# Kernel tuning notes

Measured on AMD Instinct MI355X. Metric: run time of the kernel, lower is better.

The kernel has to match this reference:

```python
import jax, jax.numpy as jnp
import numpy as np

N_NODES = 50000
N_EDGES = 1_000_000
D = 256


def gcn_conv(x, src, dst, ew, W, b, n):
    # PyG GCNConv with edge_weight: linear transform, add self-loops (w=1),
    # symmetric normalization deg^{-1/2} w deg^{-1/2}, scatter-sum, + bias.
    x = x @ W  # (n, out)
    loop = jnp.arange(n)
    src_l = jnp.concatenate([src, loop])
    dst_l = jnp.concatenate([dst, loop])
    ew_l = jnp.concatenate([ew, jnp.ones((n,), ew.dtype)])
    deg = jax.ops.segment_sum(ew_l, dst_l, num_segments=n)
    dinv = jnp.where(deg > 0, jax.lax.rsqrt(deg), 0.0).astype(x.dtype)
    norm = dinv[src_l] * ew_l * dinv[dst_l]  # (E+n,)
    out = jax.ops.segment_sum(norm[:, None] * x[src_l], dst_l, num_segments=n)
    return out + b


def setup_inputs() -> dict:
    key = jax.random.key(0)
    k = jax.random.split(key, 8)
    glorot = 1.0 / np.sqrt(D)
    return {
        "x": jax.random.normal(k[0], (N_NODES, D), jnp.float32),
        "edge_index": jax.random.randint(k[1], (2, N_EDGES), 0, N_NODES, jnp.int64),
        "edge_weight": jax.random.uniform(k[2], (N_EDGES,), jnp.float32),
        "W1": jax.random.normal(k[3], (D, D), jnp.float32) * glorot,
        "b1": jnp.zeros((D,), jnp.float32),
        "W2": jax.random.normal(k[4], (D, D), jnp.float32) * glorot,
        "b2": jnp.zeros((D,), jnp.float32),
    }


def reference(x, edge_index, edge_weight, W1, b1, W2, b2):
    n = x.shape[0]
    src, dst = edge_index[0], edge_index[1]
    h = gcn_conv(x, src, dst, edge_weight, W1, b1, n)
    h = jax.nn.relu(h)  # dropout is identity at eval
    out = gcn_conv(h, src, dst, edge_weight, W2, b2, n)
    return out
```

## Files before the change

### kernel.cpp

```cpp
#include <hip/hip_runtime.h>
#include <hip/hip_bf16.h>
#include <stdint.h>


#define D 256
#define CAP 64

typedef __attribute__((ext_vector_type(8))) short short8;
typedef __attribute__((ext_vector_type(4))) float floatx4;

__device__ inline unsigned short f2bf_rne(float f) {
    union { float f; uint32_t u; } v; v.f = f;
    uint32_t u = v.u;
    return (unsigned short)((u + 0x7FFFu + ((u >> 16) & 1u)) >> 16);
}
__device__ inline float bf_lo(uint32_t u) { union { uint32_t u; float f; } v; v.u = u << 16; return v.f; }
__device__ inline float bf_hi(uint32_t u) { union { uint32_t u; float f; } v; v.u = u & 0xFFFF0000u; return v.f; }

#define FXS 16777216.0f

#define GBM 128
#define GBN 128
#define GBK 32
#define LDA 40
#define NB_CVT 64
#define NB_P1 1600

__device__ void gemm1_block(const float* __restrict__ x, const float* __restrict__ W1,
                            unsigned short* __restrict__ C, int n, int bid,
                            unsigned char* smem) {
    unsigned short (*As)[LDA] = (unsigned short(*)[LDA])smem;
    unsigned short (*Bs)[LDA] = (unsigned short(*)[LDA])(smem + GBM * LDA * 2);
    int t = threadIdx.x;
    int bm = (bid >> 1) * GBM;
    int bn = (bid & 1) * GBN;
    int w = t >> 6, l = t & 63;
    int wm = (w >> 1) * 64, wn = (w & 1) * 64;
    int lr = l & 15;
    int lq = l >> 4;
    floatx4 acc[4][4] = {};
    for (int k0 = 0; k0 < D; k0 += GBK) {
        #pragma unroll
        for (int i = 0; i < 2; i++) {
            int c = t + i * 256;
            int row = c >> 2;
            int kk = (c & 3) * 8;
            int gr = bm + row;
            short8 av = {};
            if (gr < n) {
                const float* ap = x + (size_t)gr * D + k0 + kk;
                float4 f0 = *(const float4*)ap;
                float4 f1 = *(const float4*)(ap + 4);
                av[0] = (short)f2bf_rne(f0.x); av[1] = (short)f2bf_rne(f0.y);
                av[2] = (short)f2bf_rne(f0.z); av[3] = (short)f2bf_rne(f0.w);
                av[4] = (short)f2bf_rne(f1.x); av[5] = (short)f2bf_rne(f1.y);
                av[6] = (short)f2bf_rne(f1.z); av[7] = (short)f2bf_rne(f1.w);
            }
            *(short8*)&As[row][kk] = av;
        }
        #pragma unroll
        for (int i = 0; i < 4; i++) {
            int idx = t + i * 256;
            int kk = idx >> 5;
            int nn4 = (idx & 31) << 2;
            float4 wv = *(const float4*)(W1 + (size_t)(k0 + kk) * D + bn + nn4);
            Bs[nn4 + 0][kk] = f2bf_rne(wv.x);
            Bs[nn4 + 1][kk] = f2bf_rne(wv.y);
            Bs[nn4 + 2][kk] = f2bf_rne(wv.z);
            Bs[nn4 + 3][kk] = f2bf_rne(wv.w);
        }
        __syncthreads();
        short8 af[4], bfr[4];
        #pragma unroll
        for (int i = 0; i < 4; i++) af[i] = *(const short8*)&As[wm + i * 16 + lr][lq * 8];
        #pragma unroll
        for (int j = 0; j < 4; j++) bfr[j] = *(const short8*)&Bs[wn + j * 16 + lr][lq * 8];
        #pragma unroll
        for (int i = 0; i < 4; i++)
            #pragma unroll
            for (int j = 0; j < 4; j++)
                acc[i][j] = __builtin_amdgcn_mfma_f32_16x16x32_bf16(af[i], bfr[j], acc[i][j], 0, 0, 0);
        __syncthreads();
    }
    #pragma unroll
    for (int i = 0; i < 4; i++) {
        #pragma unroll
        for (int r = 0; r < 4; r++) {
            int row = bm + wm + i * 16 + lq * 4 + r;
            if (row >= n) continue;
            #pragma unroll
            for (int j = 0; j < 4; j++) {
                int col = bn + wn + j * 16 + lr;
                C[(size_t)row * D + col] = f2bf_rne(acc[i][j][r]);
            }
        }
    }
}

__device__ void cvtw2_block(const float* __restrict__ W2, unsigned short* __restrict__ Wt,
                            int bid, unsigned char* smem) {
    float (*sw)[33] = (float(*)[33])smem;
    int k0 = (bid >> 3) * 32, n0 = (bid & 7) * 32;
    int t = threadIdx.x;
    int tx = t & 31, ty0 = (t >> 5) * 4;
    #pragma unroll
    for (int r = 0; r < 4; r++)
        sw[ty0 + r][tx] = W2[(size_t)(k0 + ty0 + r) * D + n0 + tx];
    __syncthreads();
    #pragma unroll
    for (int r = 0; r < 4; r++)
        Wt[(size_t)(n0 + ty0 + r) * D + k0 + tx] = f2bf_rne(sw[tx][ty0 + r]);
}

__device__ void pass1_block(const int* __restrict__ src, const int* __restrict__ dst,
                            const float* __restrict__ ew,
                            unsigned long long* __restrict__ packed,
                            uint2* __restrict__ edata, int E, int bid, int nb) {
    int stride = nb * 256;
    for (int e = bid * 256 + threadIdx.x; e < E; e += stride) {
        int d = dst[e];
        float w = ew[e];
        uint32_t fx = __float2uint_rn(w * FXS);
        unsigned long long old =
            atomicAdd(&packed[(size_t)d << 3], ((unsigned long long)fx << 32) | 1ull);
        uint32_t r = (uint32_t)old;
        if (r < CAP) {
            uint2 v; v.x = (uint32_t)src[e]; v.y = __float_as_uint(w);
            edata[((size_t)d << 6) + r] = v;
        }
    }
}

__global__ __launch_bounds__(256) void fused1_kernel(const float* __restrict__ x,
                                                     const float* __restrict__ W1,
                                                     const float* __restrict__ W2,
                                                     const int* __restrict__ src,
                                                     const int* __restrict__ dst,
                                                     const float* __restrict__ ew,
                                                     unsigned short* __restrict__ xws,
                                                     unsigned short* __restrict__ w2t,
                                                     unsigned long long* __restrict__ packed,
                                                     uint2* __restrict__ edata,
                                                     int n, int E, int nb_gemm) {
    __shared__ unsigned char smem[2 * GBM * LDA * 2];
    int bid = blockIdx.x;
    if (bid < nb_gemm) {
        gemm1_block(x, W1, xws, n, bid, smem);
    } else if (bid < nb_gemm + NB_CVT) {
        cvtw2_block(W2, w2t, bid - nb_gemm, smem);
    } else {
        pass1_block(src, dst, ew, packed, edata, E, bid - nb_gemm - NB_CVT, NB_P1);
    }
}

__global__ void unpack_kernel(const unsigned long long* __restrict__ packed,
                              float* __restrict__ dinv, int n) {
    int i = blockIdx.x * 256 + threadIdx.x;
    if (i < n) {
        float deg = (float)(packed[(size_t)i << 3] >> 32) * (1.0f / FXS) + 1.0f;
        dinv[i] = rsqrtf(deg);
    }
}

__global__ __launch_bounds__(256) void gemm2_kernel(const unsigned short* __restrict__ A,
                                                    const unsigned short* __restrict__ Bt,
                                                    unsigned short* __restrict__ C, int n) {
    __shared__ unsigned short As[GBM][LDA];
    __shared__ unsigned short Bs[GBN][LDA];
    int t = threadIdx.x;
    int bm = blockIdx.x * GBM;
    int bn = blockIdx.y * GBN;
    int w = t >> 6, l = t & 63;
    int wm = (w >> 1) * 64, wn = (w & 1) * 64;
    int lr = l & 15;
    int lq = l >> 4;
    floatx4 acc[4][4] = {};
    for (int k0 = 0; k0 < D; k0 += GBK) {
        #pragma unroll
        for (int i = 0; i < 2; i++) {
            int c = t + i * 256;
            int row = c >> 2;
            int kk = (c & 3) * 8;
            int gr = bm + row;
            short8 av = {};
            if (gr < n) av = *(const short8*)&A[(size_t)gr * D + k0 + kk];
            *(short8*)&As[row][kk] = av;
            short8 bv = *(const short8*)&Bt[(size_t)(bn + row) * D + k0 + kk];
            *(short8*)&Bs[row][kk] = bv;
        }
        __syncthreads();
        short8 af[4], bfr[4];
        #pragma unroll
        for (int i = 0; i < 4; i++) af[i] = *(const short8*)&As[wm + i * 16 + lr][lq * 8];
        #pragma unroll
        for (int j = 0; j < 4; j++) bfr[j] = *(const short8*)&Bs[wn + j * 16 + lr][lq * 8];
        #pragma unroll
        for (int i = 0; i < 4; i++)
            #pragma unroll
            for (int j = 0; j < 4; j++)
                acc[i][j] = __builtin_amdgcn_mfma_f32_16x16x32_bf16(af[i], bfr[j], acc[i][j], 0, 0, 0);
        __syncthreads();
    }
    #pragma unroll
    for (int i = 0; i < 4; i++) {
        #pragma unroll
        for (int r = 0; r < 4; r++) {
            int row = bm + wm + i * 16 + lq * 4 + r;
            if (row >= n) continue;
            #pragma unroll
            for (int j = 0; j < 4; j++) {
                int col = bn + wn + j * 16 + lr;
                C[(size_t)row * D + col] = f2bf_rne(acc[i][j][r]);
            }
        }
    }
}

template <bool RELU, bool OUT_BF16>
__global__ __launch_bounds__(256) void gather_kernel(const unsigned short* __restrict__ xw,
                                                     const uint2* __restrict__ edata,
                                                     const unsigned long long* __restrict__ packed,
                                                     const float* __restrict__ dinv,
                                                     const float* __restrict__ bias,
                                                     void* __restrict__ outv, int n) {
    int wid = threadIdx.x >> 6;
    int lane = threadIdx.x & 63;
    int node = (blockIdx.x << 2) + wid;
    if (node >= n) return;
    int half = lane >> 5;
    int cl = lane & 31;
    int ch = cl << 3;
    float di = dinv[node];

    float acc[8];
    {
        uint4 r = *(const uint4*)(xw + (size_t)node * D + ch);
        float4 b0 = *(const float4*)(bias + ch);
        float4 b1 = *(const float4*)(bias + ch + 4);
        float ws = (half == 0) ? di * di : 0.0f;
        float bs = (half == 0) ? 1.0f : 0.0f;
        acc[0] = ws * bf_lo(r.x) + bs * b0.x;
        acc[1] = ws * bf_hi(r.x) + bs * b0.y;
        acc[2] = ws * bf_lo(r.y) + bs * b0.z;
        acc[3] = ws * bf_hi(r.y) + bs * b0.w;
        acc[4] = ws * bf_lo(r.z) + bs * b1.x;
        acc[5] = ws * bf_hi(r.z) + bs * b1.y;
        acc[6] = ws * bf_lo(r.w) + bs * b1.z;
        acc[7] = ws * bf_hi(r.w) + bs * b1.w;
    }

    int cnt = (int)(uint32_t)packed[(size_t)node << 3];
    cnt = min(cnt, CAP);
    const uint2* ebase = edata + ((size_t)node << 6);

    for (int j = 0; j < cnt; j += 8) {
        #pragma unroll
        for (int k = 0; k < 4; k++) {
            int e = j + 2 * k + half;
            bool valid = e < cnt;
            uint2 m; m.x = (uint32_t)node; m.y = 0u;
            if (valid) m = ebase[e];
            float co = dinv[m.x] * __uint_as_float(m.y) * di;
            uint4 r = *(const uint4*)(xw + (size_t)m.x * D + ch);
            acc[0] += co * bf_lo(r.x);
            acc[1] += co * bf_hi(r.x);
            acc[2] += co * bf_lo(r.y);
            acc[3] += co * bf_hi(r.y);
            acc[4] += co * bf_lo(r.z);
            acc[5] += co * bf_hi(r.z);
            acc[6] += co * bf_lo(r.w);
            acc[7] += co * bf_hi(r.w);
        }
    }
    #pragma unroll
    for (int k = 0; k < 8; k++) acc[k] += __shfl_xor(acc[k], 32);

    if (RELU) {
        #pragma unroll
        for (int k = 0; k < 8; k++) acc[k] = fmaxf(acc[k], 0.0f);
    }
    if (OUT_BF16) {
        if (half == 0) {
            uint4 o;
            o.x = (uint32_t)f2bf_rne(acc[0]) | ((uint32_t)f2bf_rne(acc[1]) << 16);
            o.y = (uint32_t)f2bf_rne(acc[2]) | ((uint32_t)f2bf_rne(acc[3]) << 16);
            o.z = (uint32_t)f2bf_rne(acc[4]) | ((uint32_t)f2bf_rne(acc[5]) << 16);
            o.w = (uint32_t)f2bf_rne(acc[6]) | ((uint32_t)f2bf_rne(acc[7]) << 16);
            *(uint4*)((unsigned short*)outv + (size_t)node * D + ch) = o;
        }
    } else {
        float4 o;
        int b = half * 4;
        o.x = acc[b + 0]; o.y = acc[b + 1]; o.z = acc[b + 2]; o.w = acc[b + 3];
        *(float4*)((float*)outv + (size_t)node * D + ch + b) = o;
    }
}

extern "C" void kernel_launch(void* const* d_in, const int* in_sizes, int n_in,
                              void* d_out, int out_size, void* d_ws, size_t ws_size,
                              hipStream_t stream) {
    const float* x  = (const float*)d_in[0];
    const int*   ei = (const int*)d_in[1];
    const float* ew = (const float*)d_in[2];
    const float* W1 = (const float*)d_in[3];
    const float* b1 = (const float*)d_in[4];
    const float* W2 = (const float*)d_in[5];
    const float* b2 = (const float*)d_in[6];
    float* out = (float*)d_out;

    const int n = in_sizes[0] / D;
    const int E = in_sizes[2];
    const int* src = ei;
    const int* dst = ei + E;

    char* ws = (char*)d_ws;
    size_t off = 0;
    auto carve = [&](size_t bytes) {
        char* p = ws + off;
        off = (off + bytes + 255) & ~(size_t)255;
        return p;
    };
    unsigned long long* packed = (unsigned long long*)carve((size_t)n * 64);
    float*          dinv = (float*)carve((size_t)n * 4);
    uint2*          edata = (uint2*)carve((size_t)n * CAP * 8);
    unsigned short* w2t  = (unsigned short*)carve((size_t)D * D * 2);
    unsigned short* xws  = (unsigned short*)carve((size_t)n * D * 2);
    unsigned short* hb   = (unsigned short*)carve((size_t)n * D * 2);

    const int nb_gemm = ((n + GBM - 1) / GBM) * 2;
    const int nb_node = (n + 255) / 256;

    (void)hipMemsetAsync(packed, 0, (size_t)n * 64, stream);

    fused1_kernel<<<nb_gemm + NB_CVT + NB_P1, 256, 0, stream>>>(
        x, W1, W2, src, dst, ew, xws, w2t, packed, edata, n, E, nb_gemm);

    unpack_kernel<<<nb_node, 256, 0, stream>>>(packed, dinv, n);

    dim3 agrid((n + 3) / 4);
    gather_kernel<true, true><<<agrid, 256, 0, stream>>>(xws, edata, packed, dinv, b1, hb, n);

    dim3 ggrid((n + GBM - 1) / GBM, D / GBN);
    gemm2_kernel<<<ggrid, 256, 0, stream>>>(hb, w2t, xws, n);

    gather_kernel<false, false><<<agrid, 256, 0, stream>>>(xws, edata, packed, dinv, b2, out, n);
}
```

Baseline: 362.9 us.

## Swizzle GEMM block order, vectorize W1 staging, use nontemporal stores

GEMM blocks are remapped so that groups of eight M-tiles are visited with both N-halves in sequence, which should improve L2 reuse, and gemm2 moves to a 1D grid to match. The W1 tile load now reads four rows per thread and writes packed bf16 pairs to shared memory as one 64-bit store, replacing four scalar transposed stores. Edge-data writes in pass1 and the final fp32 output writes use nontemporal stores to limit cache pollution. The risk is that strided W1 reads coalesce less well, and the nontemporal edge stores may evict data that the gather kernels later reread.

```diff
diff --git a/kernel.cpp b/kernel.cpp
--- a/kernel.cpp
+++ b/kernel.cpp
@@ -26,14 +26,30 @@
 #define NB_CVT 64
 #define NB_P1 1600
 
+__device__ inline void gemm_bmbn(int lin, int nbm, int& bm, int& bn) {
+    int full = (nbm >> 3) << 4;
+    if (lin < full) {
+        int q = lin >> 4, r = lin & 15;
+        bm = q * 8 + (r & 7);
+        bn = r >> 3;
+    } else {
+        int rr = lin - full;
+        bm = (full >> 1) + (rr >> 1);
+        bn = rr & 1;
+    }
+}
+
 __device__ void gemm1_block(const float* __restrict__ x, const float* __restrict__ W1,
                             unsigned short* __restrict__ C, int n, int bid,
                             unsigned char* smem) {
     unsigned short (*As)[LDA] = (unsigned short(*)[LDA])smem;
     unsigned short (*Bs)[LDA] = (unsigned short(*)[LDA])(smem + GBM * LDA * 2);
     int t = threadIdx.x;
-    int bm = (bid >> 1) * GBM;
-    int bn = (bid & 1) * GBN;
+    int nbm = (n + GBM - 1) / GBM;
+    int bmi, bni;
+    gemm_bmbn(bid, nbm, bmi, bni);
+    int bm = bmi * GBM;
+    int bn = bni * GBN;
     int w = t >> 6, l = t & 63;
     int wm = (w >> 1) * 64, wn = (w & 1) * 64;
     int lr = l & 15;
@@ -60,14 +76,18 @@
         }
         #pragma unroll
         for (int i = 0; i < 4; i++) {
-            int idx = t + i * 256;
-            int kk = idx >> 5;
-            int nn4 = (idx & 31) << 2;
-            float4 wv = *(const float4*)(W1 + (size_t)(k0 + kk) * D + bn + nn4);
-            Bs[nn4 + 0][kk] = f2bf_rne(wv.x);
-            Bs[nn4 + 1][kk] = f2bf_rne(wv.y);
-            Bs[nn4 + 2][kk] = f2bf_rne(wv.z);
-            Bs[nn4 + 3][kk] = f2bf_rne(wv.w);
+            int gidx = t + i * 256;
+            int nn = gidx & 127;
+            int kk = (gidx >> 7) << 2;
+            const float* wp = W1 + (size_t)(k0 + kk) * D + bn + nn;
+            float w0 = wp[0];
+            float w1 = wp[D];
+            float w2 = wp[2 * D];
+            float w3 = wp[3 * D];
+            uint32_t p0 = (uint32_t)f2bf_rne(w0) | ((uint32_t)f2bf_rne(w1) << 16);
+            uint32_t p1 = (uint32_t)f2bf_rne(w2) | ((uint32_t)f2bf_rne(w3) << 16);
+            uint2 pv; pv.x = p0; pv.y = p1;
+            *(uint2*)&Bs[nn][kk] = pv;
         }
         __syncthreads();
         short8 af[4], bfr[4];
@@ -115,7 +135,7 @@
 __device__ void pass1_block(const int* __restrict__ src, const int* __restrict__ dst,
                             const float* __restrict__ ew,
                             unsigned long long* __restrict__ packed,
-                            uint2* __restrict__ edata, int E, int bid, int nb) {
+                            unsigned long long* __restrict__ edata, int E, int bid, int nb) {
     int stride = nb * 256;
     for (int e = bid * 256 + threadIdx.x; e < E; e += stride) {
         int d = dst[e];
@@ -125,8 +145,9 @@
             atomicAdd(&packed[(size_t)d << 3], ((unsigned long long)fx << 32) | 1ull);
         uint32_t r = (uint32_t)old;
         if (r < CAP) {
-            uint2 v; v.x = (uint32_t)src[e]; v.y = __float_as_uint(w);
-            edata[((size_t)d << 6) + r] = v;
+            unsigned long long pv =
+                ((unsigned long long)__float_as_uint(w) << 32) | (uint32_t)src[e];
+            __builtin_nontemporal_store(pv, &edata[((size_t)d << 6) + r]);
         }
     }
 }
@@ -140,7 +161,7 @@
                                                      unsigned short* __restrict__ xws,
                                                      unsigned short* __restrict__ w2t,
                                                      unsigned long long* __restrict__ packed,
-                                                     uint2* __restrict__ edata,
+                                                     unsigned long long* __restrict__ edata,
                                                      int n, int E, int nb_gemm) {
     __shared__ unsigned char smem[2 * GBM * LDA * 2];
     int bid = blockIdx.x;
@@ -168,8 +189,11 @@
     __shared__ unsigned short As[GBM][LDA];
     __shared__ unsigned short Bs[GBN][LDA];
     int t = threadIdx.x;
-    int bm = blockIdx.x * GBM;
-    int bn = blockIdx.y * GBN;
+    int nbm = (n + GBM - 1) / GBM;
+    int bmi, bni;
+    gemm_bmbn(blockIdx.x, nbm, bmi, bni);
+    int bm = bmi * GBM;
+    int bn = bni * GBN;
     int w = t >> 6, l = t & 63;
     int wm = (w >> 1) * 64, wn = (w & 1) * 64;
     int lr = l & 15;
@@ -289,10 +313,10 @@
             *(uint4*)((unsigned short*)outv + (size_t)node * D + ch) = o;
         }
     } else {
-        float4 o;
+        floatx4 o;
         int b = half * 4;
-        o.x = acc[b + 0]; o.y = acc[b + 1]; o.z = acc[b + 2]; o.w = acc[b + 3];
-        *(float4*)((float*)outv + (size_t)node * D + ch + b) = o;
+        o[0] = acc[b + 0]; o[1] = acc[b + 1]; o[2] = acc[b + 2]; o[3] = acc[b + 3];
+        __builtin_nontemporal_store(o, (floatx4*)((float*)outv + (size_t)node * D + ch + b));
     }
 }
 
@@ -322,7 +346,7 @@
     };
     unsigned long long* packed = (unsigned long long*)carve((size_t)n * 64);
     float*          dinv = (float*)carve((size_t)n * 4);
-    uint2*          edata = (uint2*)carve((size_t)n * CAP * 8);
+    unsigned long long* edata = (unsigned long long*)carve((size_t)n * CAP * 8);
     unsigned short* w2t  = (unsigned short*)carve((size_t)D * D * 2);
     unsigned short* xws  = (unsigned short*)carve((size_t)n * D * 2);
     unsigned short* hb   = (unsigned short*)carve((size_t)n * D * 2);
@@ -338,10 +362,9 @@
     unpack_kernel<<<nb_node, 256, 0, stream>>>(packed, dinv, n);
 
     dim3 agrid((n + 3) / 4);
-    gather_kernel<true, true><<<agrid, 256, 0, stream>>>(xws, edata, packed, dinv, b1, hb, n);
-
-    dim3 ggrid((n + GBM - 1) / GBM, D / GBN);
-    gemm2_kernel<<<ggrid, 256, 0, stream>>>(hb, w2t, xws, n);
-
-    gather_kernel<false, false><<<agrid, 256, 0, stream>>>(xws, edata, packed, dinv, b2, out, n);
-}
+    gather_kernel<true, true><<<agrid, 256, 0, stream>>>(xws, (const uint2*)edata, packed, dinv, b1, hb, n);
+
+    gemm2_kernel<<<nb_gemm, 256, 0, stream>>>(hb, w2t, xws, n);
+
+    gather_kernel<false, false><<<agrid, 256, 0, stream>>>(xws, (const uint2*)edata, packed, dinv, b2, out, n);
+}
```

New measurement: 379.4 us. 4.5% more time.
